# Optimization experiments

Hardware: AMD Instinct MI355X
Metric: run time of the kernel (lower is better)

The kernel has to match this reference:

```python
import jax, jax.numpy as jnp
import numpy as np

NUM_HEADS = 16
SOFTPLUS_EPS = 1e-4


def rotate_half(x):
    x1, x2 = jnp.split(x, 2, axis=-1)
    return jnp.concatenate((-x2, x1), axis=-1)


def setup_inputs() -> dict:
    key = jax.random.key(0)
    B, S, H = 1, 2048, 2048
    D = H // NUM_HEADS  # 128
    ks = jax.random.split(key, 5)
    hidden_states = jax.random.normal(ks[0], (B, S, H), dtype=jnp.float32)
    # standard RoPE tables: [S, D]
    inv_freq = 1.0 / (10000.0 ** (np.arange(0, D, 2, dtype=np.float32) / D))
    freqs = np.outer(np.arange(S, dtype=np.float32), inv_freq)  # [S, D/2]
    emb = np.concatenate([freqs, freqs], axis=-1)  # [S, D]
    cos = jnp.asarray(np.cos(emb), dtype=jnp.float32)
    sin = jnp.asarray(np.sin(emb), dtype=jnp.float32)
    std = 0.02
    w_q = jax.random.normal(ks[1], (2 * H, H), dtype=jnp.float32) * std
    w_k = jax.random.normal(ks[2], (2 * H, H), dtype=jnp.float32) * std
    w_v = jax.random.normal(ks[3], (H, H), dtype=jnp.float32) * std
    w_o = jax.random.normal(ks[4], (H, H), dtype=jnp.float32) * std
    return {"hidden_states": hidden_states, "cos": cos, "sin": sin,
            "w_q": w_q, "w_k": w_k, "w_v": w_v, "w_o": w_o}


def reference(hidden_states, cos, sin, w_q, w_k, w_v, w_o):
    B, S, H = hidden_states.shape
    NH = NUM_HEADS
    D = H // NH
    # projections (torch Linear: y = x @ W.T)
    q = (hidden_states @ w_q.T).reshape(B, S, NH, 2 * D).swapaxes(1, 2)  # [B,NH,S,2D]
    k = (hidden_states @ w_k.T).reshape(B, S, NH, 2 * D).swapaxes(1, 2)
    v = (hidden_states @ w_v.T).reshape(B, S, NH, D).swapaxes(1, 2)      # [B,NH,S,D]
    q_mu, q_sigma_raw = jnp.split(q, 2, axis=-1)
    k_mu, k_sigma_raw = jnp.split(k, 2, axis=-1)
    q_sigma = jax.nn.softplus(q_sigma_raw) + SOFTPLUS_EPS
    k_sigma = jax.nn.softplus(k_sigma_raw) + SOFTPLUS_EPS
    q_w = q_mu / jnp.sqrt(q_sigma)
    k_w = k_mu / jnp.sqrt(k_sigma)
    # RoPE on variance-weighted means; cos/sin [S,D] broadcast over [B,NH,S,D]
    q_w = q_w * cos + rotate_half(q_w) * sin
    k_w = k_w * cos + rotate_half(k_w) * sin
    q_sq = jnp.sum(q_w * q_w, axis=-1, keepdims=True)          # [B,NH,S,1]
    k_sq = jnp.sum(k_w * k_w, axis=-1, keepdims=True)          # [B,NH,S,1]
    dot = jnp.einsum('bhqd,bhkd->bhqk', q_w, k_w)              # [B,NH,S,S]
    weighted_dist = q_sq + jnp.swapaxes(k_sq, -2, -1) - 2.0 * dot
    log_det_q = jnp.sum(jnp.log(q_sigma), axis=-1, keepdims=True)
    log_det_k = jnp.sum(jnp.log(k_sigma), axis=-1, keepdims=True)
    log_det = log_det_q + jnp.swapaxes(log_det_k, -2, -1)
    attn_scores = -0.5 * (weighted_dist + log_det)
    attn_probs = jax.nn.softmax(attn_scores, axis=-1)
    attn_out = jnp.einsum('bhqk,bhkd->bhqd', attn_probs, v)    # [B,NH,S,D]
    attn_out = attn_out.swapaxes(1, 2).reshape(B, S, H)
    return attn_out @ w_o.T
```

## Files before the change

### kernel.cpp

```cpp
#include <hip/hip_runtime.h>
#include <stdint.h>

#define S_LEN 2048
#define HID   2048
#define NHEAD 16
#define HD    128
#define NQK   8192
#define K_HID 2048

typedef _Float16 f16x8 __attribute__((ext_vector_type(8)));
typedef float    f32x4 __attribute__((ext_vector_type(4)));

__device__ __forceinline__ unsigned short f2h(float f) {
    _Float16 h = (_Float16)f;
    union { _Float16 h; unsigned short u; } c; c.h = h;
    return c.u;
}
__device__ __forceinline__ float h2f(unsigned short b) {
    union { unsigned short u; _Float16 h; } c; c.u = b;
    return (float)c.h;
}
__device__ __forceinline__ float softplus_f(float x) {
    return (x > 20.f) ? x : log1pf(expf(x));
}
__device__ __forceinline__ unsigned pk2h(float a, float b) {
    auto w = __builtin_amdgcn_cvt_pkrtz(a, b);
    union { decltype(w) h; unsigned u; } c; c.h = w;
    return c.u;
}
#define EXP2F(x) __builtin_amdgcn_exp2f(x)
#define LOG2E 1.44269504088896f
__device__ __forceinline__ void gload_lds16(const unsigned short* g, unsigned short* l) {
    __builtin_amdgcn_global_load_lds(
        (const __attribute__((address_space(1))) unsigned int*)g,
        (__attribute__((address_space(3))) unsigned int*)l, 16, 0, 0);
}
__device__ __forceinline__ void bar() {
    asm volatile("" ::: "memory");
    __builtin_amdgcn_s_barrier();
    asm volatile("" ::: "memory");
}
#define VMCNT(n) asm volatile("s_waitcnt vmcnt(" #n ")" ::: "memory")

__global__ __launch_bounds__(256) void cast5(const float* __restrict__ hs,
                                             const float* __restrict__ wq,
                                             const float* __restrict__ wk,
                                             const float* __restrict__ wv,
                                             const float* __restrict__ wo,
                                             unsigned short* __restrict__ hs16,
                                             unsigned short* __restrict__ wqk16,
                                             unsigned short* __restrict__ wv16,
                                             unsigned short* __restrict__ wo16) {
    int b = blockIdx.x;
    const float* src;
    unsigned short* dst;
    int i;
    if (b < 4096)       { src = hs; dst = hs16;                          i = b; }
    else if (b < 12288) { src = wq; dst = wqk16;                         i = b - 4096; }
    else if (b < 20480) { src = wk; dst = wqk16 + (size_t)4096 * K_HID;  i = b - 12288; }
    else if (b < 24576) { src = wv; dst = wv16;                          i = b - 20480; }
    else                { src = wo; dst = wo16;                          i = b - 24576; }
    int idx = i * 256 + threadIdx.x;
    float4 v = ((const float4*)src)[idx];
    ushort4 o;
    o.x = f2h(v.x); o.y = f2h(v.y); o.z = f2h(v.z); o.w = f2h(v.w);
    ((ushort4*)dst)[idx] = o;
}

template <bool OUT_F16>
__device__ __forceinline__ void gemm_body(const unsigned short* __restrict__ A,
                                          const unsigned short* __restrict__ B,
                                          void* __restrict__ Cv,
                                          int m0, int n0, int N,
                                          unsigned short* As, unsigned short* Bs) {
    const int t    = threadIdx.x;
    const int wave = t >> 6;
    const int lane = t & 63;
    const int wm   = wave >> 1, wn = wave & 1;
    const int lrow = lane & 15, quad = lane >> 4;
    const int srow = lane >> 2;
    const int scol = (lane & 3) * 8;

    f32x4 acc[4][4];
    for (int i = 0; i < 4; ++i)
        for (int j = 0; j < 4; ++j)
            acc[i][j] = (f32x4){0.f, 0.f, 0.f, 0.f};

    for (int k0 = 0; k0 < K_HID; k0 += 32) {
        for (int c = 0; c < 2; ++c) {
            int ch = wave * 2 + c;
            int row = ch * 16 + srow;
            gload_lds16(A + (size_t)(m0 + row) * K_HID + k0 + scol, &As[ch * 512]);
            gload_lds16(B + (size_t)(n0 + row) * K_HID + k0 + scol, &Bs[ch * 512]);
        }
        __syncthreads();

        f16x8 af[4], bfr[4];
        for (int tm = 0; tm < 4; ++tm)
            af[tm]  = *(const f16x8*)(&As[(wm * 64 + tm * 16 + lrow) * 32 + quad * 8]);
        for (int tn = 0; tn < 4; ++tn)
            bfr[tn] = *(const f16x8*)(&Bs[(wn * 64 + tn * 16 + lrow) * 32 + quad * 8]);
        for (int tm = 0; tm < 4; ++tm)
            for (int tn = 0; tn < 4; ++tn)
                acc[tm][tn] = __builtin_amdgcn_mfma_f32_16x16x32_f16(af[tm], bfr[tn], acc[tm][tn], 0, 0, 0);
        __syncthreads();
    }

    for (int tm = 0; tm < 4; ++tm)
        for (int tn = 0; tn < 4; ++tn) {
            int col = n0 + wn * 64 + tn * 16 + lrow;
            for (int r = 0; r < 4; ++r) {
                int row = m0 + wm * 64 + tm * 16 + quad * 4 + r;
                if (OUT_F16)
                    ((unsigned short*)Cv)[(size_t)row * N + col] = f2h(acc[tm][tn][r]);
                else
                    ((float*)Cv)[(size_t)row * N + col] = acc[tm][tn][r];
            }
        }
}

__global__ __launch_bounds__(256) void gemm_qkv(const unsigned short* __restrict__ hs16,
                                                const unsigned short* __restrict__ wqk16,
                                                const unsigned short* __restrict__ wv16,
                                                unsigned short* __restrict__ qk16,
                                                unsigned short* __restrict__ Vt) {
    __shared__ __align__(16) unsigned short As[128 * 32];
    __shared__ __align__(16) unsigned short Bs[128 * 32];
    int b = blockIdx.x;
    if (b < 1024) {
        gemm_body<true>(hs16, wqk16, qk16, (b >> 6) * 128, (b & 63) * 128, NQK, As, Bs);
    } else {
        b -= 1024;
        gemm_body<true>(wv16, hs16, Vt, (b >> 4) * 128, (b & 15) * 128, S_LEN, As, Bs);
    }
}

template <bool OUT_F16>
__global__ __launch_bounds__(256) void gemm_nt_f16(const unsigned short* __restrict__ A,
                                                   const unsigned short* __restrict__ B,
                                                   void* __restrict__ Cv,
                                                   int M, int N, int Kd) {
    __shared__ __align__(16) unsigned short As[128 * 32];
    __shared__ __align__(16) unsigned short Bs[128 * 32];
    gemm_body<OUT_F16>(A, B, Cv, blockIdx.y * 128, blockIdx.x * 128, N, As, Bs);
}

__global__ __launch_bounds__(512, 2) void gemm256_qk(const unsigned short* __restrict__ A,
                                                     const unsigned short* __restrict__ B,
                                                     unsigned short* __restrict__ C) {
    extern __shared__ __align__(16) unsigned short lds[];
    const int t    = threadIdx.x;
    const int wave = t >> 6;
    const int lane = t & 63;
    const int wm   = wave >> 2, wn = wave & 3;
    const int lrow = lane & 15, quad = lane >> 4;

    const int x  = blockIdx.x & 7;
    const int sl = blockIdx.x >> 3;
    const int tm = ((x >> 2) << 2) + (sl >> 3);
    const int tn = ((x & 3) << 3) + (sl & 7);
    const int m0 = tm << 8, n0 = tn << 8;

    const int srow = lane >> 2;
    const int scol = ((lane & 3) * 8) ^ ((lane >> 5) << 4);
    const unsigned short* Ag = A + (size_t)(m0 + wave * 16 + srow) * K_HID + scol;
    const unsigned short* Bg = B + (size_t)(n0 + wave * 16 + srow) * K_HID + scol;

    const int swz = (lrow * 32 + quad * 8) ^ ((lrow >> 3) << 4);

    f32x4 acc[8][4];
    #pragma unroll
    for (int i = 0; i < 8; ++i)
        #pragma unroll
        for (int j = 0; j < 4; ++j) acc[i][j] = (f32x4){0.f, 0.f, 0.f, 0.f};

    {
        unsigned short* la = lds + wave * 1024;
        gload_lds16(Ag,               la);
        gload_lds16(Ag + 32,          la + 512);
        gload_lds16(Ag + 262144,      la + 8192);
        gload_lds16(Ag + 262144 + 32, la + 8704);
        unsigned short* lb = la + 16384;
        gload_lds16(Bg,               lb);
        gload_lds16(Bg + 32,          lb + 512);
        gload_lds16(Bg + 262144,      lb + 8192);
        gload_lds16(Bg + 262144 + 32, lb + 8704);
    }
    VMCNT(0);
    bar();

    f16x8 ah[4][2], b01[2][2];

    const int NT = K_HID / 64;
    #pragma unroll 1
    for (int t2 = 0; t2 < NT; ++t2) {
        const int buf = t2 & 1;
        const unsigned short* Lb = lds + buf * 32768;
        unsigned short*       Ln = lds + (buf ^ 1) * 32768 + wave * 1024;
        const int k1  = (t2 + 1) * 64;
        const bool pre = (t2 < NT - 1);

        f16x8 al[4][2], b23[2][2];

        if (pre) {
            gload_lds16(Ag + k1,               Ln);
            gload_lds16(Ag + k1 + 32,          Ln + 512);
            gload_lds16(Ag + 262144 + k1,      Ln + 8192);
            gload_lds16(Ag + 262144 + k1 + 32, Ln + 8704);
        }
        #pragma unroll
        for (int i = 0; i < 4; ++i) {
            al[i][0] = *(const f16x8*)(Lb + (wm * 8 + i) * 1024 + swz);
            al[i][1] = *(const f16x8*)(Lb + (wm * 8 + i) * 1024 + 512 + swz);
        }
        if (t2) {
            __builtin_amdgcn_s_setprio(1);
            #pragma unroll
            for (int i = 0; i < 4; ++i)
                #pragma unroll
                for (int j = 0; j < 2; ++j) {
                    acc[4 + i][j] = __builtin_amdgcn_mfma_f32_16x16x32_f16(ah[i][0], b01[j][0], acc[4 + i][j], 0, 0, 0);
                    acc[4 + i][j] = __builtin_amdgcn_mfma_f32_16x16x32_f16(ah[i][1], b01[j][1], acc[4 + i][j], 0, 0, 0);
                }
            __builtin_amdgcn_s_setprio(0);
        }
        #pragma unroll
        for (int j = 0; j < 2; ++j) {
            b01[j][0] = *(const f16x8*)(Lb + 16384 + (wn * 4 + j) * 1024 + swz);
            b01[j][1] = *(const f16x8*)(Lb + 16384 + (wn * 4 + j) * 1024 + 512 + swz);
        }
        bar();

        if (pre) {
            gload_lds16(Bg + k1,               Ln + 16384);
            gload_lds16(Bg + k1 + 32,          Ln + 16896);
            gload_lds16(Bg + 262144 + k1,      Ln + 24576);
            gload_lds16(Bg + 262144 + k1 + 32, Ln + 25088);
        }
        #pragma unroll
        for (int j = 0; j < 2; ++j) {
            b23[j][0] = *(const f16x8*)(Lb + 16384 + (wn * 4 + 2 + j) * 1024 + swz);
            b23[j][1] = *(const f16x8*)(Lb + 16384 + (wn * 4 + 2 + j) * 1024 + 512 + swz);
        }
        __builtin_amdgcn_s_setprio(1);
        #pragma unroll
        for (int i = 0; i < 4; ++i)
            #pragma unroll
            for (int j = 0; j < 2; ++j) {
                acc[i][j] = __builtin_amdgcn_mfma_f32_16x16x32_f16(al[i][0], b01[j][0], acc[i][j], 0, 0, 0);
                acc[i][j] = __builtin_amdgcn_mfma_f32_16x16x32_f16(al[i][1], b01[j][1], acc[i][j], 0, 0, 0);
            }
        __builtin_amdgcn_s_setprio(0);
        bar();

        #pragma unroll
        for (int i = 0; i < 4; ++i) {
            ah[i][0] = *(const f16x8*)(Lb + (wm * 8 + 4 + i) * 1024 + swz);
            ah[i][1] = *(const f16x8*)(Lb + (wm * 8 + 4 + i) * 1024 + 512 + swz);
        }
        __builtin_amdgcn_s_setprio(1);
        #pragma unroll
        for (int i = 0; i < 4; ++i)
            #pragma unroll
            for (int j = 0; j < 2; ++j) {
                acc[i][2 + j] = __builtin_amdgcn_mfma_f32_16x16x32_f16(al[i][0], b23[j][0], acc[i][2 + j], 0, 0, 0);
                acc[i][2 + j] = __builtin_amdgcn_mfma_f32_16x16x32_f16(al[i][1], b23[j][1], acc[i][2 + j], 0, 0, 0);
            }
        __builtin_amdgcn_s_setprio(0);
        bar();

        __builtin_amdgcn_s_setprio(1);
        #pragma unroll
        for (int i = 0; i < 4; ++i)
            #pragma unroll
            for (int j = 0; j < 2; ++j) {
                acc[4 + i][2 + j] = __builtin_amdgcn_mfma_f32_16x16x32_f16(ah[i][0], b23[j][0], acc[4 + i][2 + j], 0, 0, 0);
                acc[4 + i][2 + j] = __builtin_amdgcn_mfma_f32_16x16x32_f16(ah[i][1], b23[j][1], acc[4 + i][2 + j], 0, 0, 0);
            }
        __builtin_amdgcn_s_setprio(0);
        VMCNT(0);
        bar();
    }

    __builtin_amdgcn_s_setprio(1);
    #pragma unroll
    for (int i = 0; i < 4; ++i)
        #pragma unroll
        for (int j = 0; j < 2; ++j) {
            acc[4 + i][j] = __builtin_amdgcn_mfma_f32_16x16x32_f16(ah[i][0], b01[j][0], acc[4 + i][j], 0, 0, 0);
            acc[4 + i][j] = __builtin_amdgcn_mfma_f32_16x16x32_f16(ah[i][1], b01[j][1], acc[4 + i][j], 0, 0, 0);
        }
    __builtin_amdgcn_s_setprio(0);

    #pragma unroll
    for (int m = 0; m < 8; ++m)
        #pragma unroll
        for (int n = 0; n < 4; ++n) {
            const int col = n0 + wn * 64 + n * 16 + lrow;
            #pragma unroll
            for (int r = 0; r < 4; ++r) {
                const int row = m0 + wm * 128 + m * 16 + quad * 4 + r;
                C[(size_t)row * NQK + col] = f2h(acc[m][n][r]);
            }
        }
}

__global__ __launch_bounds__(256) void prep_qk(const unsigned short* __restrict__ qk,
                                               const float* __restrict__ cosb,
                                               const float* __restrict__ sinb,
                                               unsigned short* __restrict__ Q16,
                                               unsigned short* __restrict__ K16,
                                               float* __restrict__ kbias) {
    int gid  = blockIdx.x * 4 + (threadIdx.x >> 6);
    int lane = threadIdx.x & 63;
    int h = gid >> 11;
    int s = gid & 2047;
    int d1 = lane, d2 = lane + 64;
    const unsigned short* row = qk + (size_t)s * NQK;
    float c1 = cosb[s * HD + d1], c2 = cosb[s * HD + d2];
    float s1 = sinb[s * HD + d1], s2 = sinb[s * HD + d2];
    size_t ob = ((size_t)h * S_LEN + s) * HD;

    {
        int base = h * 256;
        float mu1 = h2f(row[base + d1]),       mu2 = h2f(row[base + d2]);
        float sg1 = softplus_f(h2f(row[base + 128 + d1])) + 1e-4f;
        float sg2 = softplus_f(h2f(row[base + 128 + d2])) + 1e-4f;
        float w1 = mu1 * rsqrtf(sg1), w2 = mu2 * rsqrtf(sg2);
        float o1 = w1 * c1 - w2 * s1;
        float o2 = w2 * c2 + w1 * s2;
        Q16[ob + d1] = f2h(o1 * LOG2E);
        Q16[ob + d2] = f2h(o2 * LOG2E);
    }
    {
        int base = 4096 + h * 256;
        float mu1 = h2f(row[base + d1]),       mu2 = h2f(row[base + d2]);
        float sg1 = softplus_f(h2f(row[base + 128 + d1])) + 1e-4f;
        float sg2 = softplus_f(h2f(row[base + 128 + d2])) + 1e-4f;
        float w1 = mu1 * rsqrtf(sg1), w2 = mu2 * rsqrtf(sg2);
        float o1 = w1 * c1 - w2 * s1;
        float o2 = w2 * c2 + w1 * s2;
        unsigned short k1 = f2h(o1), k2 = f2h(o2);
        K16[ob + d1] = k1; K16[ob + d2] = k2;
        float r1 = h2f(k1), r2 = h2f(k2);
        float part = r1 * r1 + r2 * r2 + logf(sg1) + logf(sg2);
        for (int off = 32; off > 0; off >>= 1) part += __shfl_down(part, off);
        if (lane == 0) kbias[(size_t)h * S_LEN + s] = -0.5f * LOG2E * part;
    }
}

__global__ __launch_bounds__(256, 2) void flash_mfma(const unsigned short* __restrict__ Q16,
                                                     const unsigned short* __restrict__ K16,
                                                     const unsigned short* __restrict__ Vt,
                                                     const float* __restrict__ kbias,
                                                     unsigned short* __restrict__ OP,
                                                     float* __restrict__ ML) {
    constexpr int LV = 72;
    __shared__ __align__(16) unsigned short Khs[4 * 64 * 32];
    __shared__ __align__(16) unsigned short Vts[2 * 128 * 32];
    __shared__ __align__(16) unsigned short Ps[128 * LV];
    __shared__ float kb[64];

    const int t    = threadIdx.x;
    const int bb   = blockIdx.x;
    const int cc   = (bb & 7) | (((bb >> 7) & 3) << 3);
    const int h    = cc & 15;
    const int kz   = cc >> 4;
    const int q0   = ((bb >> 3) & 15) * 128;
    const int wave = t >> 6;
    const int lane = t & 63;
    const int lrow = lane & 15, quad = lane >> 4;
    const int srow = lane >> 2;
    const int scol = (lane & 3) * 8;

    f16x8 qf[2][4];
    for (int m = 0; m < 2; ++m) {
        size_t rb = ((size_t)h * S_LEN + q0 + wave * 32 + m * 16 + lrow) * HD;
        for (int kk = 0; kk < 4; ++kk)
            qf[m][kk] = *(const f16x8*)(Q16 + rb + kk * 32 + quad * 8);
    }

    float mrow[2], lsum[2];
    f32x4 Ofr[2][8];
    for (int m = 0; m < 2; ++m) { mrow[m] = -INFINITY; lsum[m] = 0.f; }
    for (int m = 0; m < 2; ++m)
        for (int d = 0; d < 8; ++d) Ofr[m][d] = (f32x4){0.f, 0.f, 0.f, 0.f};

    const int kbeg = kz * 1024;
    for (int k0 = kbeg; k0 < kbeg + 1024; k0 += 64) {
        {
            const unsigned short* kgb = K16 + ((size_t)h * S_LEN + k0) * HD;
            const unsigned short* vgb = Vt + ((size_t)h * HD) * S_LEN + k0;
            for (int c = 0; c < 4; ++c) {
                int ch = wave * 4 + c;
                int kk = ch >> 2;
                int r  = (ch & 3) * 16 + srow;
                gload_lds16(kgb + (size_t)r * HD + kk * 32 + scol, &Khs[ch * 512]);
                int kc = ch >> 3;
                int r2 = (ch & 7) * 16 + srow;
                gload_lds16(vgb + (size_t)r2 * S_LEN + kc * 32 + scol, &Vts[ch * 512]);
            }
            if (t < 64) kb[t] = kbias[(size_t)h * S_LEN + k0 + t];
        }
        __syncthreads();

        f32x4 sc[2][4];
        for (int m = 0; m < 2; ++m)
            for (int nt = 0; nt < 4; ++nt) sc[m][nt] = (f32x4){0.f, 0.f, 0.f, 0.f};
        for (int kk = 0; kk < 4; ++kk)
            for (int nt = 0; nt < 4; ++nt) {
                f16x8 khf = *(const f16x8*)(&Khs[kk * 2048 + (nt * 16 + lrow) * 32 + quad * 8]);
                sc[0][nt] = __builtin_amdgcn_mfma_f32_16x16x32_f16(khf, qf[0][kk], sc[0][nt], 0, 0, 0);
                sc[1][nt] = __builtin_amdgcn_mfma_f32_16x16x32_f16(khf, qf[1][kk], sc[1][nt], 0, 0, 0);
            }

        f32x4 kbv[4];
        #pragma unroll
        for (int nt = 0; nt < 4; ++nt)
            kbv[nt] = *(const f32x4*)(&kb[nt * 16 + quad * 4]);

        #pragma unroll
        for (int m = 0; m < 2; ++m) {
            float s[4][4];
            float mx = -INFINITY;
            #pragma unroll
            for (int nt = 0; nt < 4; ++nt)
                #pragma unroll
                for (int r = 0; r < 4; ++r) {
                    s[nt][r] = sc[m][nt][r] + kbv[nt][r];
                    mx = fmaxf(mx, s[nt][r]);
                }
            mx = fmaxf(mx, __shfl_xor(mx, 16));
            mx = fmaxf(mx, __shfl_xor(mx, 32));
            float mnew  = fmaxf(mrow[m], mx);
            float alpha = EXP2F(mrow[m] - mnew);
            mrow[m] = mnew;
            float psum = 0.f;
            unsigned pw[8];
            #pragma unroll
            for (int nt = 0; nt < 4; ++nt) {
                float p0 = EXP2F(s[nt][0] - mnew);
                float p1 = EXP2F(s[nt][1] - mnew);
                float p2 = EXP2F(s[nt][2] - mnew);
                float p3 = EXP2F(s[nt][3] - mnew);
                psum += (p0 + p1) + (p2 + p3);
                pw[nt * 2]     = pk2h(p0, p1);
                pw[nt * 2 + 1] = pk2h(p2, p3);
            }
            lsum[m] = lsum[m] * alpha + psum;
            float av0 = __shfl(alpha, quad * 4 + 0);
            float av1 = __shfl(alpha, quad * 4 + 1);
            float av2 = __shfl(alpha, quad * 4 + 2);
            float av3 = __shfl(alpha, quad * 4 + 3);
            #pragma unroll
            for (int dt = 0; dt < 8; ++dt) {
                Ofr[m][dt][0] *= av0;
                Ofr[m][dt][1] *= av1;
                Ofr[m][dt][2] *= av2;
                Ofr[m][dt][3] *= av3;
            }
            int prow = (wave * 32 + m * 16 + lrow) * LV;
            #pragma unroll
            for (int nt = 0; nt < 4; ++nt) {
                uint2 wv; wv.x = pw[nt * 2]; wv.y = pw[nt * 2 + 1];
                *(uint2*)(&Ps[prow + nt * 16 + quad * 4]) = wv;
            }
        }

        for (int c = 0; c < 2; ++c) {
            f16x8 pa0 = *(const f16x8*)(&Ps[(wave * 32 + lrow) * LV + c * 32 + quad * 8]);
            f16x8 pa1 = *(const f16x8*)(&Ps[(wave * 32 + 16 + lrow) * LV + c * 32 + quad * 8]);
            for (int dt = 0; dt < 8; ++dt) {
                f16x8 vb = *(const f16x8*)(&Vts[c * 4096 + (dt * 16 + lrow) * 32 + quad * 8]);
                Ofr[0][dt] = __builtin_amdgcn_mfma_f32_16x16x32_f16(pa0, vb, Ofr[0][dt], 0, 0, 0);
                Ofr[1][dt] = __builtin_amdgcn_mfma_f32_16x16x32_f16(pa1, vb, Ofr[1][dt], 0, 0, 0);
            }
        }
        __syncthreads();
    }

    size_t obase = (size_t)(kz * NHEAD + h) * S_LEN;
    for (int m = 0; m < 2; ++m) {
        float rs = lsum[m];
        rs += __shfl_xor(rs, 16);
        rs += __shfl_xor(rs, 32);
        if (quad == 0) {
            int qrow = q0 + wave * 32 + m * 16 + lrow;
            ML[(obase + qrow) * 2]     = mrow[m];
            ML[(obase + qrow) * 2 + 1] = rs;
        }
        for (int r = 0; r < 4; ++r) {
            int qrow = q0 + wave * 32 + m * 16 + quad * 4 + r;
            unsigned short* op = OP + (obase + qrow) * HD;
            for (int dt = 0; dt < 8; ++dt)
                op[dt * 16 + lrow] = f2h(Ofr[m][dt][r]);
        }
    }
}

__global__ __launch_bounds__(256) void flash_merge(const unsigned short* __restrict__ OP,
                                                   const float* __restrict__ ML,
                                                   unsigned short* __restrict__ Obf) {
    int row = blockIdx.x * 2 + (threadIdx.x >> 7);
    int d   = threadIdx.x & 127;
    int h = row >> 11, q = row & 2047;
    size_t i0 = (size_t)h * S_LEN + q;
    size_t i1 = (size_t)(NHEAD + h) * S_LEN + q;
    float m0 = ML[i0 * 2], l0 = ML[i0 * 2 + 1];
    float m1 = ML[i1 * 2], l1 = ML[i1 * 2 + 1];
    float mf = fmaxf(m0, m1);
    float w0 = EXP2F(m0 - mf), w1 = EXP2F(m1 - mf);
    float inv = 1.f / (l0 * w0 + l1 * w1);
    float o = (h2f(OP[i0 * HD + d]) * w0 + h2f(OP[i1 * HD + d]) * w1) * inv;
    Obf[(size_t)q * HID + h * HD + d] = f2h(o);
}

extern "C" void kernel_launch(void* const* d_in, const int* in_sizes, int n_in,
                              void* d_out, int out_size, void* d_ws, size_t ws_size,
                              hipStream_t stream) {
    const float* hs   = (const float*)d_in[0];
    const float* cosb = (const float*)d_in[1];
    const float* sinb = (const float*)d_in[2];
    const float* wq   = (const float*)d_in[3];
    const float* wk   = (const float*)d_in[4];
    const float* wv   = (const float*)d_in[5];
    const float* wo   = (const float*)d_in[6];
    float* out = (float*)d_out;
    char*  ws  = (char*)d_ws;

    unsigned short* w_qk16 = (unsigned short*)(ws);
    unsigned short* Q16    = (unsigned short*)(ws);
    unsigned short* K16    = (unsigned short*)(ws + 8388608);
    float*          kbias  = (float*)(ws + 16777216);
    unsigned short* qk16   = (unsigned short*)(ws + 33554432);
    unsigned short* OP     = (unsigned short*)(ws + 33554432);
    float*          ML     = (float*)(ws + 50331648);
    unsigned short* hs16   = (unsigned short*)(ws + 67108864);
    unsigned short* Obf    = (unsigned short*)(ws + 67108864);
    unsigned short* w_v16  = (unsigned short*)(ws + 75497472);
    unsigned short* w_o16  = (unsigned short*)(ws + 83886080);
    unsigned short* Vt     = (unsigned short*)(ws + 92274688);

    static int use256 = -1;
    if (use256 < 0) {
        hipError_t e = hipFuncSetAttribute((const void*)gemm256_qk,
                                           hipFuncAttributeMaxDynamicSharedMemorySize,
                                           131072);
        use256 = (e == hipSuccess) ? 1 : 0;
    }

    cast5<<<28672, 256, 0, stream>>>(hs, wq, wk, wv, wo, hs16, w_qk16, w_v16, w_o16);

    if (use256) {
        gemm256_qk<<<256, 512, 131072, stream>>>(hs16, w_qk16, qk16);
        gemm_nt_f16<true><<<dim3(16, 16), 256, 0, stream>>>(w_v16, hs16, Vt, HID, S_LEN, K_HID);
    } else {
        gemm_qkv<<<1280, 256, 0, stream>>>(hs16, w_qk16, w_v16, qk16, Vt);
    }

    prep_qk<<<(NHEAD * S_LEN) / 4, 256, 0, stream>>>(qk16, cosb, sinb,
                                                     Q16, K16, kbias);
    flash_mfma<<<512, 256, 0, stream>>>(Q16, K16, Vt, kbias, OP, ML);
    flash_merge<<<(NHEAD * S_LEN) / 2, 256, 0, stream>>>(OP, ML, Obf);
    gemm_nt_f16<false><<<dim3(16, 16), 256, 0, stream>>>(Obf, w_o16, out, S_LEN, HID, K_HID);
}
```

Measured before the change: 379.6 us.

## Fuse softplus, variance weighting, RoPE and key bias into QK GEMM epilogue

The 256-tile QK projection GEMM no longer writes the raw fp16 qk buffer. Instead its epilogue computes softplus and rsqrt of the sigma half through LDS, weights the mu half, applies RoPE, and writes Q/K in head-major layout plus the key bias row reduction. This removes the separate prep_qk kernel and a full round trip of the 32 MB intermediate through global memory. In exchange the epilogue gains extra barriers, LDS traffic and uncoalesced scalar stores, and the workspace is remapped.

```diff
diff --git a/kernel.cpp b/kernel.cpp
--- a/kernel.cpp
+++ b/kernel.cpp
@@ -30,6 +30,7 @@
 }
 #define EXP2F(x) __builtin_amdgcn_exp2f(x)
 #define LOG2E 1.44269504088896f
+#define LN2F  0.6931471805599453f
 __device__ __forceinline__ void gload_lds16(const unsigned short* g, unsigned short* l) {
     __builtin_amdgcn_global_load_lds(
         (const __attribute__((address_space(1))) unsigned int*)g,
@@ -147,8 +148,13 @@
 
 __global__ __launch_bounds__(512, 2) void gemm256_qk(const unsigned short* __restrict__ A,
                                                      const unsigned short* __restrict__ B,
-                                                     unsigned short* __restrict__ C) {
+                                                     const float* __restrict__ cosb,
+                                                     const float* __restrict__ sinb,
+                                                     unsigned short* __restrict__ Qo,
+                                                     unsigned short* __restrict__ Ko,
+                                                     float* __restrict__ kb_out) {
     extern __shared__ __align__(16) unsigned short lds[];
+    __shared__ float sred[3][256];
     const int t    = threadIdx.x;
     const int wave = t >> 6;
     const int lane = t & 63;
@@ -291,18 +297,105 @@
             acc[4 + i][j] = __builtin_amdgcn_mfma_f32_16x16x32_f16(ah[i][1], b01[j][1], acc[4 + i][j], 0, 0, 0);
         }
     __builtin_amdgcn_s_setprio(0);
-
-    #pragma unroll
-    for (int m = 0; m < 8; ++m)
-        #pragma unroll
-        for (int n = 0; n < 4; ++n) {
-            const int col = n0 + wn * 64 + n * 16 + lrow;
+    bar();
+
+    const int  headq = tn & 15;
+    const bool isK   = (tn >= 16);
+    float* Lf = (float*)lds;
+    const int swl = (quad & 1) << 4;
+
+    if (wn >= 2) {
+        #pragma unroll
+        for (int m = 0; m < 8; ++m)
             #pragma unroll
             for (int r = 0; r < 4; ++r) {
-                const int row = m0 + wm * 128 + m * 16 + quad * 4 + r;
-                C[(size_t)row * NQK + col] = f2h(acc[m][n][r]);
-            }
-        }
+                const int row = wm * 128 + m * 16 + quad * 4 + r;
+                float lgs = 0.f;
+                #pragma unroll
+                for (int n = 0; n < 4; ++n) {
+                    const int d = (wn - 2) * 64 + n * 16 + lrow;
+                    float xv = acc[m][n][r];
+                    float sp = (xv > 20.f) ? xv
+                             : LN2F * __log2f(1.f + EXP2F(xv * LOG2E));
+                    float sg = sp + 1e-4f;
+                    Lf[row * 128 + (d ^ swl)] = rsqrtf(sg);
+                    if (isK) lgs += __log2f(sg);
+                }
+                if (isK) {
+                    lgs += __shfl_xor(lgs, 1); lgs += __shfl_xor(lgs, 2);
+                    lgs += __shfl_xor(lgs, 4); lgs += __shfl_xor(lgs, 8);
+                    if (lrow == 0) sred[wn - 2][row] = lgs;
+                }
+            }
+    }
+    bar();
+
+    if (wn < 2) {
+        #pragma unroll
+        for (int m = 0; m < 8; ++m)
+            #pragma unroll
+            for (int n = 0; n < 4; ++n) {
+                const int d = wn * 64 + n * 16 + lrow;
+                #pragma unroll
+                for (int r = 0; r < 4; ++r) {
+                    const int row = wm * 128 + m * 16 + quad * 4 + r;
+                    float w = acc[m][n][r] * Lf[row * 128 + (d ^ swl)];
+                    acc[m][n][r] = w;
+                    const bool keep = (wn == 0) ? (m < 4) : (m >= 4);
+                    if (!keep) Lf[row * 128 + (d ^ swl)] = w;
+                }
+            }
+    }
+    bar();
+
+    if (wn < 2) {
+        const int mlo = (wn == 0) ? 0 : 4;
+        #pragma unroll
+        for (int mi = 0; mi < 4; ++mi) {
+            const int m = mlo + mi;
+            #pragma unroll
+            for (int r = 0; r < 4; ++r) {
+                const int row = wm * 128 + m * 16 + quad * 4 + r;
+                const int s   = m0 + row;
+                const size_t ob = ((size_t)headq * S_LEN + s) * HD;
+                float kq = 0.f;
+                #pragma unroll
+                for (int n = 0; n < 4; ++n) {
+                    const int dl = n * 16 + lrow;
+                    float c  = cosb[(size_t)s * HD + dl];
+                    float sn = sinb[(size_t)s * HD + dl];
+                    float wlo, whi;
+                    if (wn == 0) { wlo = acc[m][n][r]; whi = Lf[row * 128 + ((dl + 64) ^ swl)]; }
+                    else         { whi = acc[m][n][r]; wlo = Lf[row * 128 + (dl ^ swl)]; }
+                    float olo = wlo * c - whi * sn;
+                    float ohi = whi * c + wlo * sn;
+                    if (!isK) {
+                        Qo[ob + dl]      = f2h(olo * LOG2E);
+                        Qo[ob + dl + 64] = f2h(ohi * LOG2E);
+                    } else {
+                        unsigned short klo = f2h(olo), khi = f2h(ohi);
+                        Ko[ob + dl]      = klo;
+                        Ko[ob + dl + 64] = khi;
+                        float a = h2f(klo), b2 = h2f(khi);
+                        kq += a * a + b2 * b2;
+                    }
+                }
+                if (isK) {
+                    kq += __shfl_xor(kq, 1); kq += __shfl_xor(kq, 2);
+                    kq += __shfl_xor(kq, 4); kq += __shfl_xor(kq, 8);
+                    if (lrow == 0) sred[2][row] = kq;
+                }
+            }
+        }
+    }
+    if (isK) {
+        bar();
+        if (t < 256) {
+            const int row = t, s2 = m0 + row;
+            kb_out[(size_t)headq * S_LEN + s2] =
+                -0.5f * (LOG2E * sred[2][row] + sred[0][row] + sred[1][row]);
+        }
+    }
 }
 
 __global__ __launch_bounds__(256) void prep_qk(const unsigned short* __restrict__ qk,
@@ -529,14 +622,7 @@
     char*  ws  = (char*)d_ws;
 
     unsigned short* w_qk16 = (unsigned short*)(ws);
-    unsigned short* Q16    = (unsigned short*)(ws);
-    unsigned short* K16    = (unsigned short*)(ws + 8388608);
-    float*          kbias  = (float*)(ws + 16777216);
-    unsigned short* qk16   = (unsigned short*)(ws + 33554432);
-    unsigned short* OP     = (unsigned short*)(ws + 33554432);
-    float*          ML     = (float*)(ws + 50331648);
     unsigned short* hs16   = (unsigned short*)(ws + 67108864);
-    unsigned short* Obf    = (unsigned short*)(ws + 67108864);
     unsigned short* w_v16  = (unsigned short*)(ws + 75497472);
     unsigned short* w_o16  = (unsigned short*)(ws + 83886080);
     unsigned short* Vt     = (unsigned short*)(ws + 92274688);
@@ -552,15 +638,33 @@
     cast5<<<28672, 256, 0, stream>>>(hs, wq, wk, wv, wo, hs16, w_qk16, w_v16, w_o16);
 
     if (use256) {
-        gemm256_qk<<<256, 512, 131072, stream>>>(hs16, w_qk16, qk16);
+        unsigned short* OPn  = (unsigned short*)(ws);
+        float*          MLn  = (float*)(ws + 16777216);
+        unsigned short* Q16n = (unsigned short*)(ws + 33554432);
+        unsigned short* K16n = (unsigned short*)(ws + 41943040);
+        float*          kbn  = (float*)(ws + 50331648);
+        unsigned short* Obfn = (unsigned short*)(ws + 52428800);
+
+        gemm256_qk<<<256, 512, 131072, stream>>>(hs16, w_qk16, cosb, sinb,
+                                                 Q16n, K16n, kbn);
         gemm_nt_f16<true><<<dim3(16, 16), 256, 0, stream>>>(w_v16, hs16, Vt, HID, S_LEN, K_HID);
+        flash_mfma<<<512, 256, 0, stream>>>(Q16n, K16n, Vt, kbn, OPn, MLn);
+        flash_merge<<<(NHEAD * S_LEN) / 2, 256, 0, stream>>>(OPn, MLn, Obfn);
+        gemm_nt_f16<false><<<dim3(16, 16), 256, 0, stream>>>(Obfn, w_o16, out, S_LEN, HID, K_HID);
     } else {
+        unsigned short* Q16   = (unsigned short*)(ws);
+        unsigned short* K16   = (unsigned short*)(ws + 8388608);
+        float*          kbias = (float*)(ws + 16777216);
+        unsigned short* qk16  = (unsigned short*)(ws + 33554432);
+        unsigned short* OP    = (unsigned short*)(ws + 33554432);
+        float*          ML    = (float*)(ws + 50331648);
+        unsigned short* Obf   = (unsigned short*)(ws + 67108864);
+
         gemm_qkv<<<1280, 256, 0, stream>>>(hs16, w_qk16, w_v16, qk16, Vt);
-    }
-
-    prep_qk<<<(NHEAD * S_LEN) / 4, 256, 0, stream>>>(qk16, cosb, sinb,
-                                                     Q16, K16, kbias);
-    flash_mfma<<<512, 256, 0, stream>>>(Q16, K16, Vt, kbias, OP, ML);
-    flash_merge<<<(NHEAD * S_LEN) / 2, 256, 0, stream>>>(OP, ML, Obf);
-    gemm_nt_f16<false><<<dim3(16, 16), 256, 0, stream>>>(Obf, w_o16, out, S_LEN, HID, K_HID);
-}
+        prep_qk<<<(NHEAD * S_LEN) / 4, 256, 0, stream>>>(qk16, cosb, sinb,
+                                                         Q16, K16, kbias);
+        flash_mfma<<<512, 256, 0, stream>>>(Q16, K16, Vt, kbias, OP, ML);
+        flash_merge<<<(NHEAD * S_LEN) / 2, 256, 0, stream>>>(OP, ML, Obf);
+        gemm_nt_f16<false><<<dim3(16, 16), 256, 0, stream>>>(Obf, w_o16, out, S_LEN, HID, K_HID);
+    }
+}
```

New measurement: 456.8 us. 20.3% more time.

## Read K/V tiles directly from global memory instead of staging through LDS

Applied to the files above, without the earlier changes.

Removes the shared-memory staging of K, V^T and key-bias tiles in the flash attention kernel. Each wave now loads its MFMA operands straight from global memory (relying on L1/L2 caching), and the two per-iteration block barriers go away. This cuts LDS traffic and synchronisation, but every wave re-fetches the same K/V data, which multiplies global/cache traffic. The P buffer in shared memory is wave-private, so dropping the barriers stays correct.

```diff
diff --git a/kernel.cpp b/kernel.cpp
--- a/kernel.cpp
+++ b/kernel.cpp
@@ -356,10 +356,7 @@
                                                      unsigned short* __restrict__ OP,
                                                      float* __restrict__ ML) {
     constexpr int LV = 72;
-    __shared__ __align__(16) unsigned short Khs[4 * 64 * 32];
-    __shared__ __align__(16) unsigned short Vts[2 * 128 * 32];
     __shared__ __align__(16) unsigned short Ps[128 * LV];
-    __shared__ float kb[64];
 
     const int t    = threadIdx.x;
     const int bb   = blockIdx.x;
@@ -370,8 +367,6 @@
     const int wave = t >> 6;
     const int lane = t & 63;
     const int lrow = lane & 15, quad = lane >> 4;
-    const int srow = lane >> 2;
-    const int scol = (lane & 3) * 8;
 
     f16x8 qf[2][4];
     for (int m = 0; m < 2; ++m) {
@@ -386,30 +381,22 @@
     for (int m = 0; m < 2; ++m)
         for (int d = 0; d < 8; ++d) Ofr[m][d] = (f32x4){0.f, 0.f, 0.f, 0.f};
 
+    const unsigned short* Kb  = K16  + (size_t)h * S_LEN * HD;
+    const unsigned short* Vb  = Vt   + (size_t)h * HD * S_LEN;
+    const float*          kbb = kbias + (size_t)h * S_LEN;
+
     const int kbeg = kz * 1024;
     for (int k0 = kbeg; k0 < kbeg + 1024; k0 += 64) {
-        {
-            const unsigned short* kgb = K16 + ((size_t)h * S_LEN + k0) * HD;
-            const unsigned short* vgb = Vt + ((size_t)h * HD) * S_LEN + k0;
-            for (int c = 0; c < 4; ++c) {
-                int ch = wave * 4 + c;
-                int kk = ch >> 2;
-                int r  = (ch & 3) * 16 + srow;
-                gload_lds16(kgb + (size_t)r * HD + kk * 32 + scol, &Khs[ch * 512]);
-                int kc = ch >> 3;
-                int r2 = (ch & 7) * 16 + srow;
-                gload_lds16(vgb + (size_t)r2 * S_LEN + kc * 32 + scol, &Vts[ch * 512]);
-            }
-            if (t < 64) kb[t] = kbias[(size_t)h * S_LEN + k0 + t];
-        }
-        __syncthreads();
-
         f32x4 sc[2][4];
+        #pragma unroll
         for (int m = 0; m < 2; ++m)
+            #pragma unroll
             for (int nt = 0; nt < 4; ++nt) sc[m][nt] = (f32x4){0.f, 0.f, 0.f, 0.f};
+        #pragma unroll
         for (int kk = 0; kk < 4; ++kk)
+            #pragma unroll
             for (int nt = 0; nt < 4; ++nt) {
-                f16x8 khf = *(const f16x8*)(&Khs[kk * 2048 + (nt * 16 + lrow) * 32 + quad * 8]);
+                f16x8 khf = *(const f16x8*)(Kb + (size_t)(k0 + nt * 16 + lrow) * HD + kk * 32 + quad * 8);
                 sc[0][nt] = __builtin_amdgcn_mfma_f32_16x16x32_f16(khf, qf[0][kk], sc[0][nt], 0, 0, 0);
                 sc[1][nt] = __builtin_amdgcn_mfma_f32_16x16x32_f16(khf, qf[1][kk], sc[1][nt], 0, 0, 0);
             }
@@ -417,7 +404,7 @@
         f32x4 kbv[4];
         #pragma unroll
         for (int nt = 0; nt < 4; ++nt)
-            kbv[nt] = *(const f32x4*)(&kb[nt * 16 + quad * 4]);
+            kbv[nt] = *(const f32x4*)(kbb + k0 + nt * 16 + quad * 4);
 
         #pragma unroll
         for (int m = 0; m < 2; ++m) {
@@ -467,16 +454,17 @@
             }
         }
 
+        #pragma unroll
         for (int c = 0; c < 2; ++c) {
             f16x8 pa0 = *(const f16x8*)(&Ps[(wave * 32 + lrow) * LV + c * 32 + quad * 8]);
             f16x8 pa1 = *(const f16x8*)(&Ps[(wave * 32 + 16 + lrow) * LV + c * 32 + quad * 8]);
+            #pragma unroll
             for (int dt = 0; dt < 8; ++dt) {
-                f16x8 vb = *(const f16x8*)(&Vts[c * 4096 + (dt * 16 + lrow) * 32 + quad * 8]);
+                f16x8 vb = *(const f16x8*)(Vb + (size_t)(dt * 16 + lrow) * S_LEN + k0 + c * 32 + quad * 8);
                 Ofr[0][dt] = __builtin_amdgcn_mfma_f32_16x16x32_f16(pa0, vb, Ofr[0][dt], 0, 0, 0);
                 Ofr[1][dt] = __builtin_amdgcn_mfma_f32_16x16x32_f16(pa1, vb, Ofr[1][dt], 0, 0, 0);
             }
         }
-        __syncthreads();
     }
 
     size_t obase = (size_t)(kz * NHEAD + h) * S_LEN;
```

After: 454.2 us. +19.6%, slower.
